# Optimization experiments

Measured on AMD Instinct MI355X. Metric: run time of the kernel, lower is better.

## Reference

```python
import jax, jax.numpy as jnp
import numpy as np
from jax import lax

NUM_CLASSES = 2
MAX_DET = 300
SCORE_THR = 0.001
IOU_THR = 0.7
EPS = 1e-7


def _probiou_pairwise(b):
    # b: [M,5] = (cx, cy, w, h, angle). Gaussian-based rotated-box IoU (ProbIoU).
    cx, cy, w, h, t = (b[:, i] for i in range(5))
    ct, st = jnp.cos(t), jnp.sin(t)
    w2, h2 = w * w / 12.0, h * h / 12.0
    a = w2 * ct * ct + h2 * st * st
    bb = w2 * st * st + h2 * ct * ct
    c = (w2 - h2) * ct * st
    x1, y1, a1, b1, c1 = cx[:, None], cy[:, None], a[:, None], bb[:, None], c[:, None]
    x2, y2, a2, b2, c2 = cx[None, :], cy[None, :], a[None, :], bb[None, :], c[None, :]
    denom = (a1 + a2) * (b1 + b2) - (c1 + c2) ** 2 + EPS
    t1 = 0.25 * ((a1 + a2) * (y1 - y2) ** 2 + (b1 + b2) * (x1 - x2) ** 2) / denom
    t2 = 0.5 * ((c1 + c2) * (x2 - x1) * (y1 - y2)) / denom
    det1 = jnp.maximum(a1 * b1 - c1 * c1, 0.0)
    det2 = jnp.maximum(a2 * b2 - c2 * c2, 0.0)
    t3 = 0.5 * jnp.log(denom / (4.0 * jnp.sqrt(det1 * det2) + EPS) + EPS)
    bd = jnp.clip(t1 + t2 + t3, EPS, 100.0)
    hd = jnp.sqrt(1.0 - jnp.exp(-bd) + EPS)
    return 1.0 - hd


def _nms_single(boxes5, scores):
    # boxes5: [N,5], scores: [N,C] -> class-aware greedy rotated NMS
    N, C = scores.shape
    M = N * C
    cand_boxes = jnp.broadcast_to(boxes5[:, None, :], (N, C, 5)).reshape(M, 5)
    cand_scores = scores.reshape(M)
    cand_labels = jnp.broadcast_to(jnp.arange(C, dtype=jnp.int32)[None, :], (N, C)).reshape(M)
    order = jnp.argsort(-cand_scores)
    b, s, l = cand_boxes[order], cand_scores[order], cand_labels[order]
    iou = _probiou_pairwise(b)                          # [M,M]
    same = l[:, None] == l[None, :]
    sup = (iou > IOU_THR) & same
    idx = jnp.arange(M)
    valid = s > SCORE_THR

    def body(i, keep):
        row = sup[i] & (idx > i) & keep[i]
        return keep & ~row

    keep = lax.fori_loop(0, M, body, valid)
    sel = jnp.where(keep, s, -1.0)
    top = jnp.argsort(-sel)[:MAX_DET]
    ok = sel[top] > 0.0
    out_boxes = jnp.where(ok[:, None], b[top], 0.0)     # [MAX_DET,5]
    out_scores = jnp.where(ok, s[top], 0.0)             # [MAX_DET]
    out_labels = jnp.where(ok, l[top], 0)               # [MAX_DET] int32
    n_valid = jnp.minimum(jnp.sum(keep), MAX_DET).astype(jnp.int32)
    return out_boxes, out_scores, out_labels, n_valid


def _forward(x, conv_w, conv_b, bbox_w, bbox_b, cls_w, cls_b, ang_w, ang_b):
    B = x.shape[0]
    f = lax.conv_general_dilated(x, conv_w, (1, 1), 'SAME',
                                 dimension_numbers=('NCHW', 'OIHW', 'NCHW'))
    f = jax.nn.relu(f + conv_b[None, :, None, None])
    f = lax.reduce_window(f, -jnp.inf, lax.max, (1, 1, 2, 2), (1, 1, 2, 2), 'VALID')
    Hp, Wp = f.shape[2], f.shape[3]
    hw = Hp * Wp
    # 1x1-conv heads (materialized like the original), then spatial mean
    boxes = (jnp.einsum('bchw,oc->bohw', f, bbox_w) + bbox_b[None, :, None, None]
             ).reshape(B, MAX_DET, 4, hw).mean(-1)
    logits = (jnp.einsum('bchw,oc->bohw', f, cls_w) + cls_b[None, :, None, None]
              ).reshape(B, MAX_DET, NUM_CLASSES, hw).mean(-1)
    scores = jax.nn.softmax(logits, axis=2)
    angles = (jnp.einsum('bchw,oc->bohw', f, ang_w) + ang_b[None, :, None, None]
              ).reshape(B, MAX_DET, 1, hw).mean(-1)
    boxes5 = jnp.concatenate([boxes, angles], axis=-1)  # [B,300,5]
    return jax.vmap(_nms_single)(boxes5, scores)


def setup_inputs() -> dict:
    key = jax.random.key(0)
    ks = jax.random.split(key, 10)
    B, H, W = 4, 256, 256
    s = 0.1
    return {
        'x': jax.random.normal(ks[0], (B, 3, H, W), jnp.float32),
        'conv_w': jax.random.normal(ks[1], (16, 3, 3, 3), jnp.float32) * s,
        'conv_b': jax.random.normal(ks[2], (16,), jnp.float32) * s,
        'bbox_w': jax.random.normal(ks[3], (4 * MAX_DET, 16), jnp.float32) * s,
        'bbox_b': jax.random.normal(ks[4], (4 * MAX_DET,), jnp.float32) * s,
        'cls_w': jax.random.normal(ks[5], (NUM_CLASSES * MAX_DET, 16), jnp.float32) * s,
        'cls_b': jax.random.normal(ks[6], (NUM_CLASSES * MAX_DET,), jnp.float32) * s,
        'ang_w': jax.random.normal(ks[7], (MAX_DET, 16), jnp.float32) * s,
        'ang_b': jax.random.normal(ks[8], (MAX_DET,), jnp.float32) * s,
    }


def reference(x, conv_w, conv_b, bbox_w, bbox_b, cls_w, cls_b, ang_w, ang_b):
    return _forward(x, conv_w, conv_b, bbox_w, bbox_b, cls_w, cls_b, ang_w, ang_b)
```

## Files before the change

kernel.cpp:

```cpp
#include <hip/hip_runtime.h>
#include <hip/hip_bf16.h>

#define MAX_DET 300
#define NCAND 600
#define NPAD 640
#define SCORE_THR 1e-3f
#define IOU_THR 0.7f
#define EPSF 1e-7f

typedef float float4u __attribute__((ext_vector_type(4), aligned(4)));


static __device__ inline unsigned long long readlane64(unsigned long long v, int l) {
  unsigned int lo = (unsigned int)v;
  unsigned int hi = (unsigned int)(v >> 32);
  unsigned int slo = (unsigned int)__builtin_amdgcn_readlane((int)lo, l);
  unsigned int shi = (unsigned int)__builtin_amdgcn_readlane((int)hi, l);
  return ((unsigned long long)shi << 32) | (unsigned long long)slo;
}

__global__ __launch_bounds__(256) void k_conv_pool(
    const float* __restrict__ x, const float* __restrict__ cw,
    const float* __restrict__ cb, float* __restrict__ partial) {
  const int blk = blockIdx.x;
  const int chunk = blk & 15;
  const int oc = (blk >> 4) & 15;
  const int b = blk >> 8;
  const int tid = threadIdx.x;

  float w[27];
#pragma unroll
  for (int i = 0; i < 27; ++i) w[i] = cw[oc * 27 + i];
  const float bias = cb[oc];
  const float* xb = x + b * 3 * 65536;

  const int strip = chunk * 256 + tid;
  const int py = strip >> 5;
  const int x0 = (strip & 31) * 4;

  float cc0[4], cc1[4], cc2[4], cc3[4];
#pragma unroll
  for (int i = 0; i < 4; ++i) { cc0[i] = 0.f; cc1[i] = 0.f; cc2[i] = 0.f; cc3[i] = 0.f; }

#pragma unroll
  for (int ic = 0; ic < 3; ++ic) {
    const float* xc = xb + ic * 65536;
    const float* wc = w + ic * 9;
#pragma unroll
    for (int r = 0; r < 4; ++r) {
      const int y = 2 * py - 1 + r;
      if (y < 0 || y > 255) continue;
      const float* xr = xc + y * 256;
      float buf[12];
#pragma unroll
      for (int k = 0; k < 3; ++k) {
        const int c0 = 2 * x0 - 1 + 4 * k;
        if (c0 >= 0 && c0 + 3 <= 255) {
          const float4u v = *reinterpret_cast<const float4u*>(xr + c0);
          buf[4 * k + 0] = v.x; buf[4 * k + 1] = v.y;
          buf[4 * k + 2] = v.z; buf[4 * k + 3] = v.w;
        } else {
#pragma unroll
          for (int j = 0; j < 4; ++j) {
            const int c = c0 + j;
            buf[4 * k + j] = (c >= 0 && c <= 255) ? xr[c] : 0.f;
          }
        }
      }
#pragma unroll
      for (int i = 0; i < 4; ++i) {
        const float b0 = buf[2 * i], b1 = buf[2 * i + 1],
                    b2 = buf[2 * i + 2], b3 = buf[2 * i + 3];
        if (r <= 2) {
          const float w0 = wc[r * 3], w1 = wc[r * 3 + 1], w2 = wc[r * 3 + 2];
          cc0[i] += b0 * w0 + b1 * w1 + b2 * w2;
          cc1[i] += b1 * w0 + b2 * w1 + b3 * w2;
        }
        if (r >= 1) {
          const float w0 = wc[(r - 1) * 3], w1 = wc[(r - 1) * 3 + 1],
                      w2 = wc[(r - 1) * 3 + 2];
          cc2[i] += b0 * w0 + b1 * w1 + b2 * w2;
          cc3[i] += b1 * w0 + b2 * w1 + b3 * w2;
        }
      }
    }
  }

  float acc = 0.f;
#pragma unroll
  for (int i = 0; i < 4; ++i) {
    const float m = fmaxf(fmaxf(cc0[i], cc1[i]), fmaxf(cc2[i], cc3[i]));
    acc += fmaxf(m + bias, 0.f);
  }

  __shared__ float red[256];
  red[tid] = acc;
  __syncthreads();
  for (int s = 128; s > 0; s >>= 1) {
    if (tid < s) red[tid] += red[tid + s];
    __syncthreads();
  }
  if (tid == 0) partial[blk] = red[0];
}

__global__ __launch_bounds__(1024) void k_prep(
    const float* __restrict__ partial,
    const float* __restrict__ bw, const float* __restrict__ bb,
    const float* __restrict__ cwm, const float* __restrict__ cbb,
    const float* __restrict__ aw, const float* __restrict__ ab,
    float* __restrict__ boxes5, float* __restrict__ sparams,
    int* __restrict__ order_g) {
  const int b = blockIdx.x;
  const int tid = threadIdx.x;
  const int wid = tid >> 6, lane = tid & 63;

  __shared__ float fm[16];
  __shared__ float red2[256];
  __shared__ float sc[NPAD];
  __shared__ float sbox[MAX_DET * 5];
  __shared__ int order[NCAND];

  if (tid < 256) {
    const int oc = tid >> 4, j = tid & 15;
    red2[tid] = partial[(b * 16 + oc) * 16 + j];
  }
  for (int m = NCAND + tid; m < NPAD; m += 1024) sc[m] = -1e30f;
  __syncthreads();
  if (tid < 16) {
    float s = 0.f;
#pragma unroll
    for (int k = 0; k < 16; ++k) s += red2[tid * 16 + k];
    fm[tid] = s * (1.0f / 16384.0f);
  }
  __syncthreads();

  float f[16];
#pragma unroll
  for (int k = 0; k < 16; ++k) f[k] = fm[k];

  for (int o = tid; o < 4 * MAX_DET; o += 1024) {
    const float4u* wp = reinterpret_cast<const float4u*>(bw + o * 16);
    const float4u v0 = wp[0], v1 = wp[1], v2 = wp[2], v3 = wp[3];
    float wrow[16] = {v0.x, v0.y, v0.z, v0.w, v1.x, v1.y, v1.z, v1.w,
                      v2.x, v2.y, v2.z, v2.w, v3.x, v3.y, v3.z, v3.w};
    float acc = bb[o];
#pragma unroll
    for (int k = 0; k < 16; ++k) acc += wrow[k] * f[k];
    const int d = o >> 2, j = o & 3;
    sbox[d * 5 + j] = acc;
    boxes5[(b * MAX_DET + d) * 5 + j] = acc;
  }
  if (tid < MAX_DET) {
    const int o = tid;
    const float4u* wp = reinterpret_cast<const float4u*>(aw + o * 16);
    const float4u v0 = wp[0], v1 = wp[1], v2 = wp[2], v3 = wp[3];
    float wrow[16] = {v0.x, v0.y, v0.z, v0.w, v1.x, v1.y, v1.z, v1.w,
                      v2.x, v2.y, v2.z, v2.w, v3.x, v3.y, v3.z, v3.w};
    float acc = ab[o];
#pragma unroll
    for (int k = 0; k < 16; ++k) acc += wrow[k] * f[k];
    sbox[o * 5 + 4] = acc;
    boxes5[(b * MAX_DET + o) * 5 + 4] = acc;
  }
  if (tid >= 512 && tid < 512 + MAX_DET) {
    const int p = tid - 512;
    const float4u* wp0 = reinterpret_cast<const float4u*>(cwm + (2 * p) * 16);
    const float4u* wp1 = reinterpret_cast<const float4u*>(cwm + (2 * p + 1) * 16);
    const float4u u0 = wp0[0], u1 = wp0[1], u2 = wp0[2], u3 = wp0[3];
    const float4u t0 = wp1[0], t1 = wp1[1], t2 = wp1[2], t3 = wp1[3];
    float w0r[16] = {u0.x, u0.y, u0.z, u0.w, u1.x, u1.y, u1.z, u1.w,
                     u2.x, u2.y, u2.z, u2.w, u3.x, u3.y, u3.z, u3.w};
    float w1r[16] = {t0.x, t0.y, t0.z, t0.w, t1.x, t1.y, t1.z, t1.w,
                     t2.x, t2.y, t2.z, t2.w, t3.x, t3.y, t3.z, t3.w};
    float a0 = cbb[2 * p], a1 = cbb[2 * p + 1];
#pragma unroll
    for (int k = 0; k < 16; ++k) {
      a0 += w0r[k] * f[k];
      a1 += w1r[k] * f[k];
    }
    const float mx = fmaxf(a0, a1);
    const float e0 = expf(a0 - mx), e1 = expf(a1 - mx);
    const float inv = 1.f / (e0 + e1);
    sc[p * 2 + 0] = e0 * inv;
    sc[p * 2 + 1] = e1 * inv;
  }
  __syncthreads();

  float sreg[10];
#pragma unroll
  for (int k = 0; k < 10; ++k) sreg[k] = sc[k * 64 + lane];

  for (int t = 0; t < 38; ++t) {
    const int i = t * 16 + wid;
    if (i < NCAND) {
      const float si = sc[i];
      int r = 0;
#pragma unroll
      for (int k = 0; k < 10; ++k) {
        const int j = k * 64 + lane;
        const bool c = (sreg[k] > si) || (sreg[k] == si && j < i);
        r += (int)__popcll(__ballot(c));
      }
      if (lane == 0) order[r] = i;
    }
  }
  __syncthreads();

  float* P = sparams + b * 7 * NPAD;
  if (tid < NCAND) {
    const int r = tid;
    const int i = order[r];
    order_g[b * NPAD + r] = i;
    const float* bp = sbox + (i >> 1) * 5;
    const float cx = bp[0], cy = bp[1], w = bp[2], h = bp[3], t = bp[4];
    const float ct = cosf(t), st = sinf(t);
    const float w2 = w * w * (1.f / 12.f), h2 = h * h * (1.f / 12.f);
    const float a = w2 * ct * ct + h2 * st * st;
    const float bb2 = w2 * st * st + h2 * ct * ct;
    const float c = (w2 - h2) * ct * st;
    P[0 * NPAD + r] = cx;
    P[1 * NPAD + r] = cy;
    P[2 * NPAD + r] = a;
    P[3 * NPAD + r] = bb2;
    P[4 * NPAD + r] = c;
    P[5 * NPAD + r] = fmaxf(a * bb2 - c * c, 0.f);
    P[6 * NPAD + r] = sc[i];
  }
}

__global__ __launch_bounds__(256) void k_mask(
    const float* __restrict__ sparams, const int* __restrict__ order_g,
    unsigned long long* __restrict__ mask) {
  const int wid = threadIdx.x >> 6, lane = threadIdx.x & 63;
  const int g = blockIdx.x * 4 + wid;
  const int b = g / NCAND, i = g % NCAND;

  const float* P = sparams + b * 7 * NPAD;
  const int* og = order_g + b * NPAD;
  const float x1 = P[i], y1 = P[NPAD + i], a1 = P[2 * NPAD + i],
              b1 = P[3 * NPAD + i], c1 = P[4 * NPAD + i], d1 = P[5 * NPAD + i];
  const int li = og[i] & 1;

#pragma unroll
  for (int w = 0; w < 10; ++w) {
    const int j = w * 64 + lane;
    const int jc = j < NCAND ? j : NCAND - 1;
    const float x2 = P[jc], y2 = P[NPAD + jc], a2 = P[2 * NPAD + jc],
                b2 = P[3 * NPAD + jc], c2 = P[4 * NPAD + jc],
                d2 = P[5 * NPAD + jc];
    const float as = a1 + a2, bs = b1 + b2, cs = c1 + c2;
    const float dxx = x2 - x1, dyy = y1 - y2;
    const float denom = as * bs - cs * cs + EPSF;
    const float rden = 1.f / denom;
    const float t1v = 0.25f * (as * dyy * dyy + bs * dxx * dxx) * rden;
    const float t2v = 0.5f * (cs * dxx * dyy) * rden;
    const float t3v = 0.5f * logf(denom / (4.f * sqrtf(d1 * d2) + EPSF) + EPSF);
    float bd = t1v + t2v + t3v;
    bd = fminf(fmaxf(bd, EPSF), 100.f);
    const float hd = sqrtf(1.f - expf(-bd) + EPSF);
    const bool cond = (j > i) && (j < NCAND) && ((og[jc] & 1) == li) &&
                      ((1.f - hd) > IOU_THR);
    const unsigned long long mw = __ballot(cond);
    if (lane == 0) mask[(b * NCAND + i) * 10 + w] = mw;
  }
}

__global__ __launch_bounds__(1024) void k_scan(
    const float* __restrict__ boxes5, const float* __restrict__ sparams,
    const int* __restrict__ order_g, const unsigned long long* __restrict__ mask,
    float* __restrict__ out) {
  const int b = blockIdx.x;
  const int tid = threadIdx.x;
  const int wid = tid >> 6, lane = tid & 63;

  __shared__ unsigned long long m[NCAND * 10];
  __shared__ float ssc[NCAND];
  __shared__ unsigned long long keepw[10];
  __shared__ unsigned long long validbm[10];
  __shared__ unsigned long long nzbm[10];

  const unsigned long long* mg = mask + b * NCAND * 10;
  for (int k = tid; k < NCAND * 10; k += 1024) m[k] = mg[k];
  const float* P = sparams + b * 7 * NPAD;
  if (tid < NCAND) ssc[tid] = P[6 * NPAD + tid];
  __syncthreads();

  if (wid < 10) {
    const int r = wid * 64 + lane;
    bool valid = false;
    unsigned long long nzr = 0ULL;
    if (r < NCAND) {
      valid = ssc[r] > SCORE_THR;
      for (int k = 0; k < 10; ++k) nzr |= m[r * 10 + k];
    }
    const unsigned long long vb = __ballot(valid);
    const unsigned long long nb = __ballot(nzr != 0ULL);
    if (lane == 0) { validbm[wid] = vb; nzbm[wid] = nb; }
  }
  __syncthreads();

  if (tid < 64) {
    unsigned long long keep = (lane < 10) ? validbm[lane] : 0ULL;
    const unsigned long long nzv = (lane < 10) ? nzbm[lane] : 0ULL;
#pragma unroll
    for (int w = 0; w < 10; ++w) {
      unsigned long long nzs = readlane64(nzv, w);
      unsigned long long ks = readlane64(keep, w);
      while (nzs) {
        const int bit = __builtin_ctzll(nzs);
        nzs &= nzs - 1ULL;
        if ((ks >> bit) & 1ULL) {
          const int i = w * 64 + bit;
          unsigned long long row = 0ULL;
          if (lane < 10) row = m[i * 10 + lane];
          keep &= ~row;
          ks &= ~readlane64(row, w);
        }
      }
    }
    if (lane < 10) keepw[lane] = keep;
  }
  __syncthreads();

  for (int k = tid; k < MAX_DET * 5; k += 1024) out[b * MAX_DET * 5 + k] = 0.f;
  if (tid < MAX_DET) {
    out[6000 + b * MAX_DET + tid] = 0.f;
    out[7200 + b * MAX_DET + tid] = 0.f;
  }
  __syncthreads();

  const int* og = order_g + b * NPAD;
  if (tid < NCAND) {
    const int r = tid;
    const int w = r >> 6, bitp = r & 63;
    if ((keepw[w] >> bitp) & 1ULL) {
      int pos = 0;
      for (int ww = 0; ww < w; ++ww) pos += __popcll(keepw[ww]);
      pos += __popcll(keepw[w] & ((1ULL << bitp) - 1ULL));
      if (pos < MAX_DET) {
        const int i = og[r];
        const float* bp = boxes5 + (b * MAX_DET + (i >> 1)) * 5;
        float* ob = out + (b * MAX_DET + pos) * 5;
        ob[0] = bp[0]; ob[1] = bp[1]; ob[2] = bp[2]; ob[3] = bp[3]; ob[4] = bp[4];
        out[6000 + b * MAX_DET + pos] = ssc[r];
        out[7200 + b * MAX_DET + pos] = (float)(i & 1);
      }
    }
  }
  if (tid == 0) {
    int total = 0;
    for (int ww = 0; ww < 10; ++ww) total += __popcll(keepw[ww]);
    if (total > MAX_DET) total = MAX_DET;
    out[8400 + b] = (float)total;
  }
}

extern "C" void kernel_launch(void* const* d_in, const int* in_sizes, int n_in,
                              void* d_out, int out_size, void* d_ws, size_t ws_size,
                              hipStream_t stream) {
  const float* x      = (const float*)d_in[0];
  const float* conv_w = (const float*)d_in[1];
  const float* conv_b = (const float*)d_in[2];
  const float* bbox_w = (const float*)d_in[3];
  const float* bbox_b = (const float*)d_in[4];
  const float* cls_w  = (const float*)d_in[5];
  const float* cls_b  = (const float*)d_in[6];
  const float* ang_w  = (const float*)d_in[7];
  const float* ang_b  = (const float*)d_in[8];
  float* out = (float*)d_out;
  float* ws = (float*)d_ws;

  float* partial = ws;
  float* boxes5  = ws + 1024;
  float* sparams = ws + 8720;
  int*   order_g = (int*)(ws + 26640);
  unsigned long long* mask = (unsigned long long*)(ws + 29200);

  k_conv_pool<<<1024, 256, 0, stream>>>(x, conv_w, conv_b, partial);
  k_prep<<<4, 1024, 0, stream>>>(partial, bbox_w, bbox_b, cls_w, cls_b,
                                 ang_w, ang_b, boxes5, sparams, order_g);
  k_mask<<<600, 256, 0, stream>>>(sparams, order_g, mask);
  k_scan<<<4, 1024, 0, stream>>>(boxes5, sparams, order_g, mask, out);
}
```

Measured before the change: 57.92 us.

## Fuse prep into mask and scan kernels by recomputing per block

```diff
diff --git a/kernel.cpp b/kernel.cpp
--- a/kernel.cpp
+++ b/kernel.cpp
@@ -103,23 +103,13 @@
   if (tid == 0) partial[blk] = red[0];
 }
 
-__global__ __launch_bounds__(1024) void k_prep(
+static __device__ __forceinline__ void prep_local(
+    int b, int tid, int wid, int lane,
     const float* __restrict__ partial,
     const float* __restrict__ bw, const float* __restrict__ bb,
     const float* __restrict__ cwm, const float* __restrict__ cbb,
     const float* __restrict__ aw, const float* __restrict__ ab,
-    float* __restrict__ boxes5, float* __restrict__ sparams,
-    int* __restrict__ order_g) {
-  const int b = blockIdx.x;
-  const int tid = threadIdx.x;
-  const int wid = tid >> 6, lane = tid & 63;
-
-  __shared__ float fm[16];
-  __shared__ float red2[256];
-  __shared__ float sc[NPAD];
-  __shared__ float sbox[MAX_DET * 5];
-  __shared__ int order[NCAND];
-
+    float* fm, float* red2, float* sc, float* sbox, int* order) {
   if (tid < 256) {
     const int oc = tid >> 4, j = tid & 15;
     red2[tid] = partial[(b * 16 + oc) * 16 + j];
@@ -145,10 +135,9 @@
                       v2.x, v2.y, v2.z, v2.w, v3.x, v3.y, v3.z, v3.w};
     float acc = bb[o];
 #pragma unroll
-    for (int k = 0; k < 16; ++k) acc += wrow[k] * f[k];
+    for (int k = 0; k < 16; ++k) acc = fmaf(wrow[k], f[k], acc);
     const int d = o >> 2, j = o & 3;
     sbox[d * 5 + j] = acc;
-    boxes5[(b * MAX_DET + d) * 5 + j] = acc;
   }
   if (tid < MAX_DET) {
     const int o = tid;
@@ -158,9 +147,8 @@
                       v2.x, v2.y, v2.z, v2.w, v3.x, v3.y, v3.z, v3.w};
     float acc = ab[o];
 #pragma unroll
-    for (int k = 0; k < 16; ++k) acc += wrow[k] * f[k];
+    for (int k = 0; k < 16; ++k) acc = fmaf(wrow[k], f[k], acc);
     sbox[o * 5 + 4] = acc;
-    boxes5[(b * MAX_DET + o) * 5 + 4] = acc;
   }
   if (tid >= 512 && tid < 512 + MAX_DET) {
     const int p = tid - 512;
@@ -175,8 +163,8 @@
     float a0 = cbb[2 * p], a1 = cbb[2 * p + 1];
 #pragma unroll
     for (int k = 0; k < 16; ++k) {
-      a0 += w0r[k] * f[k];
-      a1 += w1r[k] * f[k];
+      a0 = fmaf(w0r[k], f[k], a0);
+      a1 = fmaf(w1r[k], f[k], a1);
     }
     const float mx = fmaxf(a0, a1);
     const float e0 = expf(a0 - mx), e1 = expf(a1 - mx);
@@ -205,12 +193,32 @@
     }
   }
   __syncthreads();
-
-  float* P = sparams + b * 7 * NPAD;
+}
+
+__global__ __launch_bounds__(1024) void k_mask(
+    const float* __restrict__ partial,
+    const float* __restrict__ bw, const float* __restrict__ bb,
+    const float* __restrict__ cwm, const float* __restrict__ cbb,
+    const float* __restrict__ aw, const float* __restrict__ ab,
+    unsigned long long* __restrict__ mask) {
+  const int blk = blockIdx.x;
+  const int b = blk / 38, rg = blk % 38;
+  const int tid = threadIdx.x;
+  const int wid = tid >> 6, lane = tid & 63;
+
+  __shared__ float fm[16];
+  __shared__ float red2[256];
+  __shared__ float sc[NPAD];
+  __shared__ float sbox[MAX_DET * 5];
+  __shared__ int order[NCAND];
+  __shared__ float sx[NCAND], sy[NCAND], sA[NCAND], sB[NCAND], sC[NCAND],
+      sD[NCAND];
+
+  prep_local(b, tid, wid, lane, partial, bw, bb, cwm, cbb, aw, ab,
+             fm, red2, sc, sbox, order);
+
   if (tid < NCAND) {
-    const int r = tid;
-    const int i = order[r];
-    order_g[b * NPAD + r] = i;
+    const int i = order[tid];
     const float* bp = sbox + (i >> 1) * 5;
     const float cx = bp[0], cy = bp[1], w = bp[2], h = bp[3], t = bp[4];
     const float ct = cosf(t), st = sinf(t);
@@ -218,61 +226,55 @@
     const float a = w2 * ct * ct + h2 * st * st;
     const float bb2 = w2 * st * st + h2 * ct * ct;
     const float c = (w2 - h2) * ct * st;
-    P[0 * NPAD + r] = cx;
-    P[1 * NPAD + r] = cy;
-    P[2 * NPAD + r] = a;
-    P[3 * NPAD + r] = bb2;
-    P[4 * NPAD + r] = c;
-    P[5 * NPAD + r] = fmaxf(a * bb2 - c * c, 0.f);
-    P[6 * NPAD + r] = sc[i];
-  }
-}
-
-__global__ __launch_bounds__(256) void k_mask(
-    const float* __restrict__ sparams, const int* __restrict__ order_g,
-    unsigned long long* __restrict__ mask) {
-  const int wid = threadIdx.x >> 6, lane = threadIdx.x & 63;
-  const int g = blockIdx.x * 4 + wid;
-  const int b = g / NCAND, i = g % NCAND;
-
-  const float* P = sparams + b * 7 * NPAD;
-  const int* og = order_g + b * NPAD;
-  const float x1 = P[i], y1 = P[NPAD + i], a1 = P[2 * NPAD + i],
-              b1 = P[3 * NPAD + i], c1 = P[4 * NPAD + i], d1 = P[5 * NPAD + i];
-  const int li = og[i] & 1;
-
-#pragma unroll
-  for (int w = 0; w < 10; ++w) {
-    const int j = w * 64 + lane;
-    const int jc = j < NCAND ? j : NCAND - 1;
-    const float x2 = P[jc], y2 = P[NPAD + jc], a2 = P[2 * NPAD + jc],
-                b2 = P[3 * NPAD + jc], c2 = P[4 * NPAD + jc],
-                d2 = P[5 * NPAD + jc];
-    const float as = a1 + a2, bs = b1 + b2, cs = c1 + c2;
-    const float dxx = x2 - x1, dyy = y1 - y2;
-    const float denom = as * bs - cs * cs + EPSF;
-    const float rden = 1.f / denom;
-    const float t1v = 0.25f * (as * dyy * dyy + bs * dxx * dxx) * rden;
-    const float t2v = 0.5f * (cs * dxx * dyy) * rden;
-    const float t3v = 0.5f * logf(denom / (4.f * sqrtf(d1 * d2) + EPSF) + EPSF);
-    float bd = t1v + t2v + t3v;
-    bd = fminf(fmaxf(bd, EPSF), 100.f);
-    const float hd = sqrtf(1.f - expf(-bd) + EPSF);
-    const bool cond = (j > i) && (j < NCAND) && ((og[jc] & 1) == li) &&
-                      ((1.f - hd) > IOU_THR);
-    const unsigned long long mw = __ballot(cond);
-    if (lane == 0) mask[(b * NCAND + i) * 10 + w] = mw;
+    sx[tid] = cx; sy[tid] = cy; sA[tid] = a; sB[tid] = bb2; sC[tid] = c;
+    sD[tid] = fmaxf(a * bb2 - c * c, 0.f);
+  }
+  __syncthreads();
+
+  const int i = rg * 16 + wid;
+  if (i < NCAND) {
+    const float x1 = sx[i], y1 = sy[i], a1 = sA[i], b1 = sB[i], c1 = sC[i],
+                d1 = sD[i];
+    const int li = order[i] & 1;
+#pragma unroll
+    for (int w = 0; w < 10; ++w) {
+      const int j = w * 64 + lane;
+      const int jc = j < NCAND ? j : NCAND - 1;
+      const float x2 = sx[jc], y2 = sy[jc], a2 = sA[jc], b2 = sB[jc],
+                  c2 = sC[jc], d2 = sD[jc];
+      const float as = a1 + a2, bs = b1 + b2, cs = c1 + c2;
+      const float dxx = x2 - x1, dyy = y1 - y2;
+      const float denom = as * bs - cs * cs + EPSF;
+      const float rden = 1.f / denom;
+      const float t1v = 0.25f * (as * dyy * dyy + bs * dxx * dxx) * rden;
+      const float t2v = 0.5f * (cs * dxx * dyy) * rden;
+      const float t3v = 0.5f * logf(denom / (4.f * sqrtf(d1 * d2) + EPSF) + EPSF);
+      float bd = t1v + t2v + t3v;
+      bd = fminf(fmaxf(bd, EPSF), 100.f);
+      const float hd = sqrtf(1.f - expf(-bd) + EPSF);
+      const bool cond = (j > i) && (j < NCAND) && ((order[jc] & 1) == li) &&
+                        ((1.f - hd) > IOU_THR);
+      const unsigned long long mw = __ballot(cond);
+      if (lane == 0) mask[(b * NCAND + i) * 10 + w] = mw;
+    }
   }
 }
 
 __global__ __launch_bounds__(1024) void k_scan(
-    const float* __restrict__ boxes5, const float* __restrict__ sparams,
-    const int* __restrict__ order_g, const unsigned long long* __restrict__ mask,
-    float* __restrict__ out) {
+    const float* __restrict__ partial,
+    const float* __restrict__ bw, const float* __restrict__ bb,
+    const float* __restrict__ cwm, const float* __restrict__ cbb,
+    const float* __restrict__ aw, const float* __restrict__ ab,
+    const unsigned long long* __restrict__ mask, float* __restrict__ out) {
   const int b = blockIdx.x;
   const int tid = threadIdx.x;
   const int wid = tid >> 6, lane = tid & 63;
 
+  __shared__ float fm[16];
+  __shared__ float red2[256];
+  __shared__ float sc[NPAD];
+  __shared__ float sbox[MAX_DET * 5];
+  __shared__ int order[NCAND];
   __shared__ unsigned long long m[NCAND * 10];
   __shared__ float ssc[NCAND];
   __shared__ unsigned long long keepw[10];
@@ -281,8 +283,11 @@
 
   const unsigned long long* mg = mask + b * NCAND * 10;
   for (int k = tid; k < NCAND * 10; k += 1024) m[k] = mg[k];
-  const float* P = sparams + b * 7 * NPAD;
-  if (tid < NCAND) ssc[tid] = P[6 * NPAD + tid];
+
+  prep_local(b, tid, wid, lane, partial, bw, bb, cwm, cbb, aw, ab,
+             fm, red2, sc, sbox, order);
+
+  if (tid < NCAND) ssc[tid] = sc[order[tid]];
   __syncthreads();
 
   if (wid < 10) {
@@ -329,7 +334,6 @@
   }
   __syncthreads();
 
-  const int* og = order_g + b * NPAD;
   if (tid < NCAND) {
     const int r = tid;
     const int w = r >> 6, bitp = r & 63;
@@ -338,8 +342,8 @@
       for (int ww = 0; ww < w; ++ww) pos += __popcll(keepw[ww]);
       pos += __popcll(keepw[w] & ((1ULL << bitp) - 1ULL));
       if (pos < MAX_DET) {
-        const int i = og[r];
-        const float* bp = boxes5 + (b * MAX_DET + (i >> 1)) * 5;
+        const int i = order[r];
+        const float* bp = sbox + (i >> 1) * 5;
         float* ob = out + (b * MAX_DET + pos) * 5;
         ob[0] = bp[0]; ob[1] = bp[1]; ob[2] = bp[2]; ob[3] = bp[3]; ob[4] = bp[4];
         out[6000 + b * MAX_DET + pos] = ssc[r];
@@ -371,14 +375,11 @@
   float* ws = (float*)d_ws;
 
   float* partial = ws;
-  float* boxes5  = ws + 1024;
-  float* sparams = ws + 8720;
-  int*   order_g = (int*)(ws + 26640);
   unsigned long long* mask = (unsigned long long*)(ws + 29200);
 
   k_conv_pool<<<1024, 256, 0, stream>>>(x, conv_w, conv_b, partial);
-  k_prep<<<4, 1024, 0, stream>>>(partial, bbox_w, bbox_b, cls_w, cls_b,
-                                 ang_w, ang_b, boxes5, sparams, order_g);
-  k_mask<<<600, 256, 0, stream>>>(sparams, order_g, mask);
-  k_scan<<<4, 1024, 0, stream>>>(boxes5, sparams, order_g, mask, out);
-}
+  k_mask<<<152, 1024, 0, stream>>>(partial, bbox_w, bbox_b, cls_w, cls_b,
+                                   ang_w, ang_b, mask);
+  k_scan<<<4, 1024, 0, stream>>>(partial, bbox_w, bbox_b, cls_w, cls_b,
+                                 ang_w, ang_b, mask, out);
+}
```

Measured after the change: 85.50 us. +47.6%, slower.
